# Performance work log

Hardware: AMD Instinct MI355X
Metric: run time of the kernel (lower is better)

## Reference

```python
import jax, jax.numpy as jnp
import numpy as np
from jax.scipy.special import gammaln

D_MODEL = 256
N_HEADS = 8
BIAS_HIDDEN = 64
B, N = 2, 1024
EPS = 1e-4


def setup_inputs() -> dict:
    key = jax.random.key(0)
    ks = jax.random.split(key, 12)
    d, h = D_MODEL, BIAS_HIDDEN
    s = 0.02
    return {
        "src": jax.random.normal(ks[0], (B, N, d), jnp.float32),
        "coords": jax.random.normal(ks[1], (B, N, 4), jnp.float32),
        "Wq": jax.random.normal(ks[2], (d, d), jnp.float32) * s,
        "Wk": jax.random.normal(ks[3], (d, d), jnp.float32) * s,
        "Wv": jax.random.normal(ks[4], (d, d), jnp.float32) * s,
        "Wo": jax.random.normal(ks[5], (d, d), jnp.float32) * s,
        "gw1": jax.random.normal(ks[6], (h, 2), jnp.float32) * s,
        "gb1": jnp.zeros((h,), jnp.float32),
        "gw2": jax.random.normal(ks[7], (1, h), jnp.float32) * s,
        "gb2": jnp.zeros((1,), jnp.float32),
        "dw1": jax.random.normal(ks[8], (h, 4), jnp.float32) * s,
        "db1": jnp.zeros((h,), jnp.float32),
        "dw2": jax.random.normal(ks[9], (2, h), jnp.float32) * s,
        "db2": jnp.zeros((2,), jnp.float32),
    }


def reference(src, coords, Wq, Wk, Wv, Wo, gw1, gb1, gw2, gb2, dw1, db1, dw2, db2):
    Bb, Nn, d = src.shape
    H = N_HEADS
    dh = d // H
    scale = 1.0 / np.sqrt(dh).astype(np.float32)

    def split_heads(x):  # [B,N,d] -> [B,H,N,dh]
        return x.reshape(Bb, Nn, H, dh).transpose(0, 2, 1, 3)

    q = split_heads(src @ Wq.T)
    k = split_heads(src @ Wk.T)
    v = split_heads(src @ Wv.T)

    attn = jnp.einsum("bhnd,bhmd->bhnm", q, k) * scale  # [B,H,N,N]

    xyz = coords[..., :3]
    t = coords[..., 3]
    delta = xyz[:, :, None, :] - xyz[:, None, :, :]        # [B,N,N,3]
    dist = jnp.linalg.norm(delta, axis=-1)                  # [B,N,N]
    dt = t[:, :, None] - t[:, None, :]                      # [B,N,N]

    # geometric bias MLP: 2 -> hidden -> 1
    geom_feat = jnp.stack((dist, dt), axis=-1)              # [B,N,N,2]
    gh = jax.nn.relu(geom_feat @ gw1.T + gb1)
    bias = (gh @ gw2.T + gb2)[..., 0]                       # [B,N,N]

    # delay bias MLP: [dist, xyz_j] (4) -> hidden -> 2 (Gamma shape, rate)
    xyz_j = jnp.broadcast_to(xyz[:, None, :, :], (Bb, Nn, Nn, 3))
    delay_feat = jnp.concatenate((dist[..., None], xyz_j), axis=-1)  # [B,N,N,4]
    dhid = jax.nn.relu(delay_feat @ dw1.T + db1)
    raw = dhid @ dw2.T + db2                                # [B,N,N,2]
    shape = jax.nn.softplus(raw[..., 0]) + EPS
    rate = jax.nn.softplus(raw[..., 1]) + EPS
    dt_pos = jnp.maximum(jnp.abs(dt), EPS)
    # Gamma(shape, rate).log_prob(x)
    log_prob = (shape * jnp.log(rate) + (shape - 1.0) * jnp.log(dt_pos)
                - rate * dt_pos - gammaln(shape))
    bias = bias + log_prob

    attn = attn + bias[:, None, :, :]
    weights = jax.nn.softmax(attn, axis=-1)
    out = jnp.einsum("bhnm,bhmd->bhnd", weights, v)
    out = out.transpose(0, 2, 1, 3).reshape(Bb, Nn, d)
    return out @ Wo.T
```

## Files before the change

kernel.cpp:

```cpp
#include <hip/hip_runtime.h>
#include <hip/hip_bf16.h>
#include <math.h>

constexpr int B_ = 2;
constexpr int N_ = 1024;
constexpr int D_ = 256;
constexpr int H_ = 8;
constexpr int DH_ = 32;
constexpr float SCALE_ = 0.17677669529663687f;
constexpr float LOG2E_ = 1.4426950408889634f;
constexpr float SCALE2_ = SCALE_ * LOG2E_;
constexpr float EPSV_ = 1e-4f;

typedef __attribute__((ext_vector_type(8))) short short8;
typedef __attribute__((ext_vector_type(4))) float f32x4;

__device__ __forceinline__ unsigned short f2bf(float x) {
  __hip_bfloat16 h = __float2bfloat16(x);
  return __builtin_bit_cast(unsigned short, h);
}
__device__ __forceinline__ float bf2f(unsigned short u) {
  unsigned int x = ((unsigned int)u) << 16;
  return __builtin_bit_cast(float, x);
}

__device__ __forceinline__ float lgamma_fast(float x) {
  float y = (x < 1.f) ? x : (x - 1.f);
  float g = fmaf(y, 0.035868343f, -0.193527818f);
  g = fmaf(y, g, 0.482199394f);
  g = fmaf(y, g, -0.756704078f);
  g = fmaf(y, g, 0.918206857f);
  g = fmaf(y, g, -0.897056937f);
  g = fmaf(y, g, 0.988205891f);
  g = fmaf(y, g, -0.577191652f);
  g = fmaf(y, g, 1.0f);
  float lg = __logf(g);
  return (x < 1.f) ? lg - __logf(x) : lg;
}
__device__ __forceinline__ float softplus_fast(float x) {
  return __logf(1.f + __expf(x));
}

__global__ __launch_bounds__(256)
void prep_kernel(const float* __restrict__ coords,
                 const float* __restrict__ gw1, const float* __restrict__ gb1,
                 const float* __restrict__ gw2, const float* __restrict__ gb2,
                 const float* __restrict__ dw1, const float* __restrict__ db1,
                 const float* __restrict__ dw2, const float* __restrict__ db2,
                 const float* __restrict__ Wq, const float* __restrict__ Wk,
                 const float* __restrict__ Wv, const float* __restrict__ Wo,
                 const float* __restrict__ src,
                 unsigned short* __restrict__ whi, unsigned short* __restrict__ wlo,
                 unsigned short* __restrict__ shi, unsigned short* __restrict__ slo,
                 float2* __restrict__ Gp, float4* __restrict__ Dp) {
  const int tid = threadIdx.x;
  const int bi = blockIdx.x;

  if (bi < 33) {
    int e = bi * 256 + tid;
    if (e < 129 * 64) {
      int kv = e >> 6, ku = e & 63;
      float v = kv * 0.25f - 16.0f;
      float u0 = ku * 0.25f, u1 = u0 + 0.25f;
      float a0 = gb2[0], a1 = gb2[0];
#pragma unroll 4
      for (int h = 0; h < 64; ++h) {
        float g0 = gw1[2 * h], g1 = gw1[2 * h + 1], gb = gb1[h], g2 = gw2[h];
        float base = fmaf(g1, v, gb);
        a0 = fmaf(g2, fmaxf(fmaf(g0, u0, base), 0.f), a0);
        a1 = fmaf(g2, fmaxf(fmaf(g0, u1, base), 0.f), a1);
      }
      Gp[e] = make_float2(a0, a1);
    }
    return;
  }

  if (bi < 545) {
    int t = (bi - 33) * 256 + tid;
    int b = t >> 16;
    int rem = t & 65535;
    int k = rem >> 10;
    int j = rem & 1023;
    float4 cj = ((const float4*)coords)[b * N_ + j];
    float u0 = k * 0.25f, u1 = u0 + 0.25f;
    float r00 = db2[0], r10 = db2[1], r01 = db2[0], r11 = db2[1];
#pragma unroll 4
    for (int h = 0; h < 64; ++h) {
      float w0 = dw1[4 * h], wx = dw1[4 * h + 1], wy = dw1[4 * h + 2], wz = dw1[4 * h + 3];
      float c0 = db1[h], c1 = dw2[h], c2 = dw2[64 + h];
      float dp = fmaf(wx, cj.x, fmaf(wy, cj.y, fmaf(wz, cj.z, c0)));
      float h0 = fmaxf(fmaf(w0, u0, dp), 0.f);
      float h1 = fmaxf(fmaf(w0, u1, dp), 0.f);
      r00 = fmaf(c1, h0, r00); r10 = fmaf(c2, h0, r10);
      r01 = fmaf(c1, h1, r01); r11 = fmaf(c2, h1, r11);
    }
    Dp[((size_t)b * 64 + k) * 1024 + j] = make_float4(r00, r10, r01, r11);
    return;
  }

  if (bi < 609) {
    int idx = ((bi - 545) * 256 + tid) * 16;
    int m = idx >> 16;
    int off = idx & 65535;
    const float* p = ((m == 0) ? Wq : (m == 1) ? Wk : (m == 2) ? Wv : Wo) + off;
    unsigned short* dhi = whi + idx;
    unsigned short* dlo = wlo + idx;
#pragma unroll
    for (int q = 0; q < 4; ++q) {
      float4 f = *(const float4*)(p + q * 4);
      ushort4 hi, lo;
      hi.x = f2bf(f.x); lo.x = f2bf(f.x - bf2f(hi.x));
      hi.y = f2bf(f.y); lo.y = f2bf(f.y - bf2f(hi.y));
      hi.z = f2bf(f.z); lo.z = f2bf(f.z - bf2f(hi.z));
      hi.w = f2bf(f.w); lo.w = f2bf(f.w - bf2f(hi.w));
      *(ushort4*)(dhi + q * 4) = hi;
      *(ushort4*)(dlo + q * 4) = lo;
    }
    return;
  }

  {
    int idx = ((bi - 609) * 256 + tid) * 16;
    const float* p = src + idx;
    unsigned short* dhi = shi + idx;
    unsigned short* dlo = slo + idx;
#pragma unroll
    for (int q = 0; q < 4; ++q) {
      float4 f = *(const float4*)(p + q * 4);
      ushort4 hi, lo;
      hi.x = f2bf(f.x); lo.x = f2bf(f.x - bf2f(hi.x));
      hi.y = f2bf(f.y); lo.y = f2bf(f.y - bf2f(hi.y));
      hi.z = f2bf(f.z); lo.z = f2bf(f.z - bf2f(hi.z));
      hi.w = f2bf(f.w); lo.w = f2bf(f.w - bf2f(hi.w));
      *(ushort4*)(dhi + q * 4) = hi;
      *(ushort4*)(dlo + q * 4) = lo;
    }
  }
}

__device__ __forceinline__
void mfma_wave_pure(const unsigned short* __restrict__ Ahi,
                    const unsigned short* __restrict__ Alo,
                    const unsigned short* __restrict__ whi,
                    const unsigned short* __restrict__ wlo,
                    int r0, int c0, f32x4 (&acc)[4]) {
  const int l = threadIdx.x & 63;
  const int lr = l & 15, lg = l >> 4;
#pragma unroll
  for (int ct = 0; ct < 4; ++ct) acc[ct] = (f32x4){0.f, 0.f, 0.f, 0.f};
#pragma unroll 2
  for (int ks = 0; ks < 8; ++ks) {
    size_t aoff = (size_t)(r0 + lr) * D_ + ks * 32 + lg * 8;
    short8 ahi = *(const short8*)(Ahi + aoff);
    short8 alo = *(const short8*)(Alo + aoff);
#pragma unroll
    for (int ct = 0; ct < 4; ++ct) {
      size_t woff = (size_t)(c0 + ct * 16 + lr) * D_ + ks * 32 + lg * 8;
      short8 wh = *(const short8*)(whi + woff);
      short8 wl = *(const short8*)(wlo + woff);
      acc[ct] = __builtin_amdgcn_mfma_f32_16x16x32_bf16(ahi, wh, acc[ct], 0, 0, 0);
      acc[ct] = __builtin_amdgcn_mfma_f32_16x16x32_bf16(alo, wh, acc[ct], 0, 0, 0);
      acc[ct] = __builtin_amdgcn_mfma_f32_16x16x32_bf16(ahi, wl, acc[ct], 0, 0, 0);
    }
  }
}

__global__ __launch_bounds__(256)
void fused1_kernel(const float* __restrict__ coords,
                   const float2* __restrict__ Gp, const float4* __restrict__ Dp,
                   float* __restrict__ bias,
                   const unsigned short* __restrict__ shi,
                   const unsigned short* __restrict__ slo,
                   const unsigned short* __restrict__ whi,
                   const unsigned short* __restrict__ wlo,
                   unsigned short* __restrict__ qbf, unsigned short* __restrict__ kbf,
                   unsigned short* __restrict__ vtbf) {
  const int tid = threadIdx.x;
  const int bi = blockIdx.x;

  if (bi >= 2048) {
    const int bi2 = bi - 2048;
    const int z = bi2 >> 7;
    const int rem = bi2 & 127;
    const int by = rem >> 5, bx = rem & 31;
    const int w = tid >> 6;
    const int r0 = bx * 64 + w * 16;
    const int c0 = by * 64;
    f32x4 acc[4];
    mfma_wave_pure(shi, slo, whi + z * 65536, wlo + z * 65536, r0, c0, acc);

    const int l = tid & 63, lr = l & 15, lg = l >> 4;
    if (z < 2) {
      unsigned short* dst = (z == 0) ? qbf : kbf;
#pragma unroll
      for (int ct = 0; ct < 4; ++ct) {
        int o = c0 + ct * 16 + lr, h = o >> 5, d = o & 31;
#pragma unroll
        for (int r = 0; r < 4; ++r) {
          int R = r0 + lg * 4 + r, b = R >> 10, n = R & 1023;
          dst[(size_t)((b * H_ + h) * N_ + n) * DH_ + d] = f2bf(acc[ct][r]);
        }
      }
    } else {
#pragma unroll
      for (int ct = 0; ct < 4; ++ct) {
        int o = c0 + ct * 16 + lr, h = o >> 5, d = o & 31;
#pragma unroll
        for (int r = 0; r < 4; ++r) {
          int R = r0 + lg * 4 + r, b = R >> 10, n = R & 1023;
          vtbf[(size_t)((b * H_ + h) * DH_ + d) * N_ + n] = f2bf(acc[ct][r]);
        }
      }
    }
    return;
  }

  const int jt = bi & 3;
  const int it = (bi >> 2) & 255;
  const int b  = bi >> 10;
  const int j  = jt * 256 + tid;
  const int ibase = it * 4;

  const float4 cj = ((const float4*)coords)[b * N_ + j];
  const float4* DpB = Dp + (size_t)b * 64 * 1024;

#pragma unroll
  for (int ii = 0; ii < 4; ++ii) {
    const float* cp = coords + 4 * (b * N_ + ibase + ii);
    float dx = cp[0] - cj.x, dy = cp[1] - cj.y, dz = cp[2] - cj.z;
    float dist = sqrtf(dx * dx + dy * dy + dz * dz);
    float dtv = cp[3] - cj.w;

    float uf = fminf(dist, 15.999f) * 4.0f;
    int ku = (int)uf;
    float fu = uf - (float)ku;
    float4 t = DpB[(size_t)ku * 1024 + j];
    float raw0 = fmaf(fu, t.z - t.x, t.x);
    float raw1 = fmaf(fu, t.w - t.y, t.y);

    float vf = (fminf(fmaxf(dtv, -16.0f), 15.999f) + 16.0f) * 4.0f;
    int kv = (int)vf;
    float fv = vf - (float)kv;
    float2 a = Gp[kv * 64 + ku];
    float2 c = Gp[(kv + 1) * 64 + ku];
    float gl = fmaf(fu, a.y - a.x, a.x);
    float gh = fmaf(fu, c.y - c.x, c.x);
    float biasg = fmaf(fv, gh - gl, gl);

    float sh  = softplus_fast(raw0) + EPSV_;
    float ra  = softplus_fast(raw1) + EPSV_;
    float dtp = fmaxf(fabsf(dtv), EPSV_);
    float lp  = sh * __logf(ra) + (sh - 1.f) * __logf(dtp) - ra * dtp - lgamma_fast(sh);
    bias[(size_t)(b * N_ + ibase + ii) * N_ + j] = (biasg + lp) * LOG2E_;
  }
}

__global__ __launch_bounds__(512)
void attn_kernel(const unsigned short* __restrict__ qbf,
                 const unsigned short* __restrict__ kbf,
                 const unsigned short* __restrict__ vtbf,
                 const float* __restrict__ biasg,
                 unsigned short* __restrict__ ophi,
                 unsigned short* __restrict__ oplo) {
  __shared__ __align__(16) unsigned short p_lds[8][16][72];
  __shared__ float acc_lds[3][2][16][32];
  __shared__ float ml_lds[3][2][16][2];

  const int tid = threadIdx.x;
  const int w = tid >> 6, l = tid & 63;
  const int s = w >> 2, jq = w & 3;
  const int lr = l & 15, lg = l >> 4;
  const int bh = blockIdx.x >> 5;
  const int qb = blockIdx.x & 31;
  const int b = bh >> 3, h = bh & 7;
  const int ibase = qb * 32 + s * 16;

  const short8 ones8 = {16256, 16256, 16256, 16256, 16256, 16256, 16256, 16256};

  const short8 qfrag =
      *(const short8*)(qbf + (size_t)(bh * N_ + ibase + lr) * DH_ + lg * 8);
  const unsigned short* kb = kbf + (size_t)bh * N_ * DH_;
  const unsigned short* vb = vtbf + (size_t)bh * DH_ * N_;
  const float* bbase = biasg + (size_t)b * N_ * N_;

  f32x4 acc[2], accL;
  acc[0] = (f32x4){0.f, 0.f, 0.f, 0.f};
  acc[1] = (f32x4){0.f, 0.f, 0.f, 0.f};
  accL   = (f32x4){0.f, 0.f, 0.f, 0.f};
  float m_run[4];
#pragma unroll
  for (int r = 0; r < 4; ++r) m_run[r] = -3e38f;

  const int jbeg = jq * 256;
  for (int j0 = jbeg; j0 < jbeg + 256; j0 += 64) {
    f32x4 sc[4];
#pragma unroll
    for (int t = 0; t < 4; ++t) {
      short8 kf = *(const short8*)(kb + (size_t)(j0 + t * 16 + lr) * DH_ + lg * 8);
      sc[t] = __builtin_amdgcn_mfma_f32_16x16x32_bf16(
          qfrag, kf, (f32x4){0.f, 0.f, 0.f, 0.f}, 0, 0, 0);
    }
#pragma unroll
    for (int r = 0; r < 4; ++r) {
      const float* bp = bbase + (size_t)(ibase + lg * 4 + r) * N_ + j0 + lr;
#pragma unroll
      for (int t = 0; t < 4; ++t)
        sc[t][r] = fmaf(sc[t][r], SCALE2_, bp[t * 16]);
    }
    float mt[4];
#pragma unroll
    for (int r = 0; r < 4; ++r)
      mt[r] = fmaxf(fmaxf(sc[0][r], sc[1][r]), fmaxf(sc[2][r], sc[3][r]));
#pragma unroll
    for (int off = 1; off < 16; off <<= 1)
#pragma unroll
      for (int r = 0; r < 4; ++r)
        mt[r] = fmaxf(mt[r], __shfl_xor(mt[r], off));
    float corr[4];
#pragma unroll
    for (int r = 0; r < 4; ++r) {
      float mn = fmaxf(m_run[r], mt[r]);
      corr[r] = exp2f(m_run[r] - mn);
      m_run[r] = mn;
    }
#pragma unroll
    for (int t = 0; t < 4; ++t)
#pragma unroll
      for (int r = 0; r < 4; ++r)
        sc[t][r] = exp2f(sc[t][r] - m_run[r]);
#pragma unroll
    for (int r = 0; r < 4; ++r) {
      acc[0][r] *= corr[r];
      acc[1][r] *= corr[r];
      accL[r]   *= corr[r];
    }
#pragma unroll
    for (int t = 0; t < 4; ++t)
#pragma unroll
      for (int r = 0; r < 4; ++r)
        p_lds[w][lg * 4 + r][t * 16 + lr] = f2bf(sc[t][r]);
#pragma unroll
    for (int kc = 0; kc < 2; ++kc) {
      short8 pf = *(const short8*)&p_lds[w][lr][kc * 32 + lg * 8];
#pragma unroll
      for (int c = 0; c < 2; ++c) {
        short8 vf = *(const short8*)(vb + (size_t)(c * 16 + lr) * N_ +
                                     j0 + kc * 32 + lg * 8);
        acc[c] = __builtin_amdgcn_mfma_f32_16x16x32_bf16(pf, vf, acc[c], 0, 0, 0);
      }
      accL = __builtin_amdgcn_mfma_f32_16x16x32_bf16(pf, ones8, accL, 0, 0, 0);
    }
  }

  if (jq > 0) {
#pragma unroll
    for (int c = 0; c < 2; ++c)
#pragma unroll
      for (int r = 0; r < 4; ++r)
        acc_lds[jq - 1][s][lg * 4 + r][c * 16 + lr] = acc[c][r];
    if (lr == 0) {
#pragma unroll
      for (int r = 0; r < 4; ++r) {
        ml_lds[jq - 1][s][lg * 4 + r][0] = m_run[r];
        ml_lds[jq - 1][s][lg * 4 + r][1] = accL[r];
      }
    }
  }
  __syncthreads();
  if (jq == 0) {
    float c0[4], cq[3][4], linv[4];
#pragma unroll
    for (int r = 0; r < 4; ++r) {
      int row = lg * 4 + r;
      float m = m_run[r];
#pragma unroll
      for (int q = 0; q < 3; ++q) m = fmaxf(m, ml_lds[q][s][row][0]);
      c0[r] = exp2f(m_run[r] - m);
      float lsum = accL[r] * c0[r];
#pragma unroll
      for (int q = 0; q < 3; ++q) {
        cq[q][r] = exp2f(ml_lds[q][s][row][0] - m);
        lsum = fmaf(ml_lds[q][s][row][1], cq[q][r], lsum);
      }
      linv[r] = 1.f / lsum;
    }
#pragma unroll
    for (int c = 0; c < 2; ++c) {
#pragma unroll
      for (int r = 0; r < 4; ++r) {
        int row = lg * 4 + r;
        int i = ibase + row;
        int d = c * 16 + lr;
        float o = acc[c][r] * c0[r];
#pragma unroll
        for (int q = 0; q < 3; ++q)
          o = fmaf(acc_lds[q][s][row][d], cq[q][r], o);
        o *= linv[r];
        size_t oidx = (size_t)(b * N_ + i) * D_ + h * DH_ + d;
        unsigned short hi = f2bf(o);
        ophi[oidx] = hi;
        oplo[oidx] = f2bf(o - bf2f(hi));
      }
    }
  }
}

__global__ __launch_bounds__(256)
void projo_kernel(const unsigned short* __restrict__ ophi,
                  const unsigned short* __restrict__ oplo,
                  const unsigned short* __restrict__ whi,
                  const unsigned short* __restrict__ wlo,
                  float* __restrict__ out) {
  const int w = threadIdx.x >> 6;
  const int r0 = blockIdx.x * 64 + w * 16;
  const int c0 = blockIdx.y * 64;
  f32x4 acc[4];
  mfma_wave_pure(ophi, oplo, whi + 3 * 65536, wlo + 3 * 65536, r0, c0, acc);
  const int l = threadIdx.x & 63, lr = l & 15, lg = l >> 4;
#pragma unroll
  for (int ct = 0; ct < 4; ++ct)
#pragma unroll
    for (int r = 0; r < 4; ++r)
      out[(size_t)(r0 + lg * 4 + r) * D_ + c0 + ct * 16 + lr] = acc[ct][r];
}

extern "C" void kernel_launch(void* const* d_in, const int* in_sizes, int n_in,
                              void* d_out, int out_size, void* d_ws, size_t ws_size,
                              hipStream_t stream) {
  const float* src    = (const float*)d_in[0];
  const float* coords = (const float*)d_in[1];
  const float* Wq  = (const float*)d_in[2];
  const float* Wk  = (const float*)d_in[3];
  const float* Wv  = (const float*)d_in[4];
  const float* Wo  = (const float*)d_in[5];
  const float* gw1 = (const float*)d_in[6];
  const float* gb1 = (const float*)d_in[7];
  const float* gw2 = (const float*)d_in[8];
  const float* gb2 = (const float*)d_in[9];
  const float* dw1 = (const float*)d_in[10];
  const float* db1 = (const float*)d_in[11];
  const float* dw2 = (const float*)d_in[12];
  const float* db2 = (const float*)d_in[13];
  float* out = (float*)d_out;

  char* wsb = (char*)d_ws;
  unsigned short* qbf  = (unsigned short*)wsb;
  unsigned short* kbf  = (unsigned short*)(wsb + (1 << 20));
  unsigned short* vtbf = (unsigned short*)(wsb + (2 << 20));
  float* biasw         = (float*)(wsb + (3 << 20));
  unsigned short* whi  = (unsigned short*)(wsb + (11 << 20));
  unsigned short* wlo  = (unsigned short*)(wsb + (11 << 20) + (512 << 10));
  unsigned short* shi  = (unsigned short*)(wsb + (12 << 20));
  unsigned short* slo  = (unsigned short*)(wsb + (13 << 20));
  unsigned short* ophi = (unsigned short*)(wsb + (14 << 20));
  unsigned short* oplo = (unsigned short*)(wsb + (15 << 20));
  float2* Gp           = (float2*)(wsb + (16 << 20));
  float4* Dp           = (float4*)(wsb + (17 << 20));

  prep_kernel<<<737, 256, 0, stream>>>(coords, gw1, gb1, gw2, gb2,
                                       dw1, db1, dw2, db2,
                                       Wq, Wk, Wv, Wo, src,
                                       whi, wlo, shi, slo, Gp, Dp);
  fused1_kernel<<<2432, 256, 0, stream>>>(coords, Gp, Dp, biasw,
                                          shi, slo, whi, wlo, qbf, kbf, vtbf);
  attn_kernel<<<512, 512, 0, stream>>>(qbf, kbf, vtbf, biasw, ophi, oplo);
  projo_kernel<<<dim3(32, 4), 256, 0, stream>>>(ophi, oplo, whi, wlo, out);
}
```

Baseline: 71.25 us.

## Fuse attention and output projection via software grid barrier

Merges the attention kernel and the output-projection kernel into one launch. A global atomic barrier separates the two phases, and the first 64 blocks then run the projection. This removes one kernel launch and the gap between kernels. In exchange it adds a memset launch and spin-wait synchronisation. It also relies on all 512 blocks being co-resident, which is risky if occupancy does not allow it.

```diff
diff --git a/kernel.cpp b/kernel.cpp
--- a/kernel.cpp
+++ b/kernel.cpp
@@ -11,6 +11,7 @@
 constexpr float LOG2E_ = 1.4426950408889634f;
 constexpr float SCALE2_ = SCALE_ * LOG2E_;
 constexpr float EPSV_ = 1e-4f;
+constexpr unsigned GRID2_ = 512;
 
 typedef __attribute__((ext_vector_type(8))) short short8;
 typedef __attribute__((ext_vector_type(4))) float f32x4;
@@ -39,6 +40,22 @@
 }
 __device__ __forceinline__ float softplus_fast(float x) {
   return __logf(1.f + __expf(x));
+}
+
+__device__ __forceinline__ void grid_barrier(unsigned* bar) {
+  __syncthreads();
+  if (threadIdx.x == 0) {
+    __threadfence();
+    unsigned old = atomicAdd(bar, 1u);
+    if (old == GRID2_ - 1) {
+      atomicExch(bar + 1, 1u);
+    } else {
+      while (atomicAdd(bar + 1, 0u) == 0u)
+        __builtin_amdgcn_s_sleep(2);
+    }
+    __threadfence();
+  }
+  __syncthreads();
 }
 
 __global__ __launch_bounds__(256)
@@ -143,8 +160,7 @@
                     const unsigned short* __restrict__ Alo,
                     const unsigned short* __restrict__ whi,
                     const unsigned short* __restrict__ wlo,
-                    int r0, int c0, f32x4 (&acc)[4]) {
-  const int l = threadIdx.x & 63;
+                    int r0, int c0, int l, f32x4 (&acc)[4]) {
   const int lr = l & 15, lg = l >> 4;
 #pragma unroll
   for (int ct = 0; ct < 4; ++ct) acc[ct] = (f32x4){0.f, 0.f, 0.f, 0.f};
@@ -187,7 +203,7 @@
     const int r0 = bx * 64 + w * 16;
     const int c0 = by * 64;
     f32x4 acc[4];
-    mfma_wave_pure(shi, slo, whi + z * 65536, wlo + z * 65536, r0, c0, acc);
+    mfma_wave_pure(shi, slo, whi + z * 65536, wlo + z * 65536, r0, c0, tid & 63, acc);
 
     const int l = tid & 63, lr = l & 15, lg = l >> 4;
     if (z < 2) {
@@ -255,173 +271,181 @@
   }
 }
 
-__global__ __launch_bounds__(512)
-void attn_kernel(const unsigned short* __restrict__ qbf,
-                 const unsigned short* __restrict__ kbf,
-                 const unsigned short* __restrict__ vtbf,
-                 const float* __restrict__ biasg,
-                 unsigned short* __restrict__ ophi,
-                 unsigned short* __restrict__ oplo) {
+__global__
+__attribute__((amdgpu_flat_work_group_size(512, 512), amdgpu_waves_per_eu(4, 4)))
+void attn_projo_kernel(const unsigned short* __restrict__ qbf,
+                       const unsigned short* __restrict__ kbf,
+                       const unsigned short* __restrict__ vtbf,
+                       const float* __restrict__ biasg,
+                       const unsigned short* __restrict__ whi,
+                       const unsigned short* __restrict__ wlo,
+                       unsigned short* __restrict__ ophi,
+                       unsigned short* __restrict__ oplo,
+                       float* __restrict__ out,
+                       unsigned* __restrict__ bar) {
   __shared__ __align__(16) unsigned short p_lds[8][16][72];
   __shared__ float acc_lds[3][2][16][32];
   __shared__ float ml_lds[3][2][16][2];
 
   const int tid = threadIdx.x;
-  const int w = tid >> 6, l = tid & 63;
-  const int s = w >> 2, jq = w & 3;
-  const int lr = l & 15, lg = l >> 4;
-  const int bh = blockIdx.x >> 5;
-  const int qb = blockIdx.x & 31;
-  const int b = bh >> 3, h = bh & 7;
-  const int ibase = qb * 32 + s * 16;
-
-  const short8 ones8 = {16256, 16256, 16256, 16256, 16256, 16256, 16256, 16256};
-
-  const short8 qfrag =
-      *(const short8*)(qbf + (size_t)(bh * N_ + ibase + lr) * DH_ + lg * 8);
-  const unsigned short* kb = kbf + (size_t)bh * N_ * DH_;
-  const unsigned short* vb = vtbf + (size_t)bh * DH_ * N_;
-  const float* bbase = biasg + (size_t)b * N_ * N_;
-
-  f32x4 acc[2], accL;
-  acc[0] = (f32x4){0.f, 0.f, 0.f, 0.f};
-  acc[1] = (f32x4){0.f, 0.f, 0.f, 0.f};
-  accL   = (f32x4){0.f, 0.f, 0.f, 0.f};
-  float m_run[4];
-#pragma unroll
-  for (int r = 0; r < 4; ++r) m_run[r] = -3e38f;
-
-  const int jbeg = jq * 256;
-  for (int j0 = jbeg; j0 < jbeg + 256; j0 += 64) {
-    f32x4 sc[4];
-#pragma unroll
-    for (int t = 0; t < 4; ++t) {
-      short8 kf = *(const short8*)(kb + (size_t)(j0 + t * 16 + lr) * DH_ + lg * 8);
-      sc[t] = __builtin_amdgcn_mfma_f32_16x16x32_bf16(
-          qfrag, kf, (f32x4){0.f, 0.f, 0.f, 0.f}, 0, 0, 0);
-    }
-#pragma unroll
-    for (int r = 0; r < 4; ++r) {
-      const float* bp = bbase + (size_t)(ibase + lg * 4 + r) * N_ + j0 + lr;
+  const int bi = blockIdx.x;
+
+  {
+    const int w = tid >> 6, l = tid & 63;
+    const int s = w >> 2, jq = w & 3;
+    const int lr = l & 15, lg = l >> 4;
+    const int bh = bi >> 5;
+    const int qb = bi & 31;
+    const int b = bh >> 3, h = bh & 7;
+    const int ibase = qb * 32 + s * 16;
+
+    const short8 ones8 = {16256, 16256, 16256, 16256, 16256, 16256, 16256, 16256};
+    const short8 qfrag =
+        *(const short8*)(qbf + (size_t)(bh * N_ + ibase + lr) * DH_ + lg * 8);
+    const unsigned short* kb = kbf + (size_t)bh * N_ * DH_;
+    const unsigned short* vb = vtbf + (size_t)bh * DH_ * N_;
+    const float* bbase = biasg + (size_t)b * N_ * N_;
+
+    f32x4 acc[2], accL;
+    acc[0] = (f32x4){0.f, 0.f, 0.f, 0.f};
+    acc[1] = (f32x4){0.f, 0.f, 0.f, 0.f};
+    accL   = (f32x4){0.f, 0.f, 0.f, 0.f};
+    float m_run[4];
+#pragma unroll
+    for (int r = 0; r < 4; ++r) m_run[r] = -3e38f;
+
+    const int jbeg = jq * 256;
+    for (int j0 = jbeg; j0 < jbeg + 256; j0 += 64) {
+      f32x4 sc[4];
+#pragma unroll
+      for (int t = 0; t < 4; ++t) {
+        short8 kf = *(const short8*)(kb + (size_t)(j0 + t * 16 + lr) * DH_ + lg * 8);
+        sc[t] = __builtin_amdgcn_mfma_f32_16x16x32_bf16(
+            qfrag, kf, (f32x4){0.f, 0.f, 0.f, 0.f}, 0, 0, 0);
+      }
+#pragma unroll
+      for (int r = 0; r < 4; ++r) {
+        const float* bp = bbase + (size_t)(ibase + lg * 4 + r) * N_ + j0 + lr;
+#pragma unroll
+        for (int t = 0; t < 4; ++t)
+          sc[t][r] = fmaf(sc[t][r], SCALE2_, bp[t * 16]);
+      }
+      float mt[4];
+#pragma unroll
+      for (int r = 0; r < 4; ++r)
+        mt[r] = fmaxf(fmaxf(sc[0][r], sc[1][r]), fmaxf(sc[2][r], sc[3][r]));
+#pragma unroll
+      for (int off = 1; off < 16; off <<= 1)
+#pragma unroll
+        for (int r = 0; r < 4; ++r)
+          mt[r] = fmaxf(mt[r], __shfl_xor(mt[r], off));
+      float corr[4];
+#pragma unroll
+      for (int r = 0; r < 4; ++r) {
+        float mn = fmaxf(m_run[r], mt[r]);
+        corr[r] = exp2f(m_run[r] - mn);
+        m_run[r] = mn;
+      }
 #pragma unroll
       for (int t = 0; t < 4; ++t)
-        sc[t][r] = fmaf(sc[t][r], SCALE2_, bp[t * 16]);
-    }
-    float mt[4];
-#pragma unroll
-    for (int r = 0; r < 4; ++r)
-      mt[r] = fmaxf(fmaxf(sc[0][r], sc[1][r]), fmaxf(sc[2][r], sc[3][r]));
-#pragma unroll
-    for (int off = 1; off < 16; off <<= 1)
-#pragma unroll
-      for (int r = 0; r < 4; ++r)
-        mt[r] = fmaxf(mt[r], __shfl_xor(mt[r], off));
-    float corr[4];
-#pragma unroll
-    for (int r = 0; r < 4; ++r) {
-      float mn = fmaxf(m_run[r], mt[r]);
-      corr[r] = exp2f(m_run[r] - mn);
-      m_run[r] = mn;
-    }
-#pragma unroll
-    for (int t = 0; t < 4; ++t)
-#pragma unroll
-      for (int r = 0; r < 4; ++r)
-        sc[t][r] = exp2f(sc[t][r] - m_run[r]);
-#pragma unroll
-    for (int r = 0; r < 4; ++r) {
-      acc[0][r] *= corr[r];
-      acc[1][r] *= corr[r];
-      accL[r]   *= corr[r];
-    }
-#pragma unroll
-    for (int t = 0; t < 4; ++t)
-#pragma unroll
-      for (int r = 0; r < 4; ++r)
-        p_lds[w][lg * 4 + r][t * 16 + lr] = f2bf(sc[t][r]);
-#pragma unroll
-    for (int kc = 0; kc < 2; ++kc) {
-      short8 pf = *(const short8*)&p_lds[w][lr][kc * 32 + lg * 8];
-#pragma unroll
-      for (int c = 0; c < 2; ++c) {
-        short8 vf = *(const short8*)(vb + (size_t)(c * 16 + lr) * N_ +
-                                     j0 + kc * 32 + lg * 8);
-        acc[c] = __builtin_amdgcn_mfma_f32_16x16x32_bf16(pf, vf, acc[c], 0, 0, 0);
-      }
-      accL = __builtin_amdgcn_mfma_f32_16x16x32_bf16(pf, ones8, accL, 0, 0, 0);
-    }
-  }
-
-  if (jq > 0) {
-#pragma unroll
-    for (int c = 0; c < 2; ++c)
-#pragma unroll
-      for (int r = 0; r < 4; ++r)
-        acc_lds[jq - 1][s][lg * 4 + r][c * 16 + lr] = acc[c][r];
-    if (lr == 0) {
+#pragma unroll
+        for (int r = 0; r < 4; ++r)
+          sc[t][r] = exp2f(sc[t][r] - m_run[r]);
 #pragma unroll
       for (int r = 0; r < 4; ++r) {
-        ml_lds[jq - 1][s][lg * 4 + r][0] = m_run[r];
-        ml_lds[jq - 1][s][lg * 4 + r][1] = accL[r];
-      }
-    }
-  }
-  __syncthreads();
-  if (jq == 0) {
-    float c0[4], cq[3][4], linv[4];
-#pragma unroll
-    for (int r = 0; r < 4; ++r) {
-      int row = lg * 4 + r;
-      float m = m_run[r];
-#pragma unroll
-      for (int q = 0; q < 3; ++q) m = fmaxf(m, ml_lds[q][s][row][0]);
-      c0[r] = exp2f(m_run[r] - m);
-      float lsum = accL[r] * c0[r];
-#pragma unroll
-      for (int q = 0; q < 3; ++q) {
-        cq[q][r] = exp2f(ml_lds[q][s][row][0] - m);
-        lsum = fmaf(ml_lds[q][s][row][1], cq[q][r], lsum);
-      }
-      linv[r] = 1.f / lsum;
-    }
-#pragma unroll
-    for (int c = 0; c < 2; ++c) {
+        acc[0][r] *= corr[r];
+        acc[1][r] *= corr[r];
+        accL[r]   *= corr[r];
+      }
+#pragma unroll
+      for (int t = 0; t < 4; ++t)
+#pragma unroll
+        for (int r = 0; r < 4; ++r)
+          p_lds[w][lg * 4 + r][t * 16 + lr] = f2bf(sc[t][r]);
+#pragma unroll
+      for (int kc = 0; kc < 2; ++kc) {
+        short8 pf = *(const short8*)&p_lds[w][lr][kc * 32 + lg * 8];
+#pragma unroll
+        for (int c = 0; c < 2; ++c) {
+          short8 vf = *(const short8*)(vb + (size_t)(c * 16 + lr) * N_ +
+                                       j0 + kc * 32 + lg * 8);
+          acc[c] = __builtin_amdgcn_mfma_f32_16x16x32_bf16(pf, vf, acc[c], 0, 0, 0);
+        }
+        accL = __builtin_amdgcn_mfma_f32_16x16x32_bf16(pf, ones8, accL, 0, 0, 0);
+      }
+    }
+
+    if (jq > 0) {
+#pragma unroll
+      for (int c = 0; c < 2; ++c)
+#pragma unroll
+        for (int r = 0; r < 4; ++r)
+          acc_lds[jq - 1][s][lg * 4 + r][c * 16 + lr] = acc[c][r];
+      if (lr == 0) {
+#pragma unroll
+        for (int r = 0; r < 4; ++r) {
+          ml_lds[jq - 1][s][lg * 4 + r][0] = m_run[r];
+          ml_lds[jq - 1][s][lg * 4 + r][1] = accL[r];
+        }
+      }
+    }
+    __syncthreads();
+    if (jq == 0) {
+      float c0[4], cq[3][4], linv[4];
 #pragma unroll
       for (int r = 0; r < 4; ++r) {
         int row = lg * 4 + r;
-        int i = ibase + row;
-        int d = c * 16 + lr;
-        float o = acc[c][r] * c0[r];
-#pragma unroll
-        for (int q = 0; q < 3; ++q)
-          o = fmaf(acc_lds[q][s][row][d], cq[q][r], o);
-        o *= linv[r];
-        size_t oidx = (size_t)(b * N_ + i) * D_ + h * DH_ + d;
-        unsigned short hi = f2bf(o);
-        ophi[oidx] = hi;
-        oplo[oidx] = f2bf(o - bf2f(hi));
-      }
-    }
-  }
-}
-
-__global__ __launch_bounds__(256)
-void projo_kernel(const unsigned short* __restrict__ ophi,
-                  const unsigned short* __restrict__ oplo,
-                  const unsigned short* __restrict__ whi,
-                  const unsigned short* __restrict__ wlo,
-                  float* __restrict__ out) {
-  const int w = threadIdx.x >> 6;
-  const int r0 = blockIdx.x * 64 + w * 16;
-  const int c0 = blockIdx.y * 64;
-  f32x4 acc[4];
-  mfma_wave_pure(ophi, oplo, whi + 3 * 65536, wlo + 3 * 65536, r0, c0, acc);
-  const int l = threadIdx.x & 63, lr = l & 15, lg = l >> 4;
-#pragma unroll
-  for (int ct = 0; ct < 4; ++ct)
-#pragma unroll
-    for (int r = 0; r < 4; ++r)
-      out[(size_t)(r0 + lg * 4 + r) * D_ + c0 + ct * 16 + lr] = acc[ct][r];
+        float m = m_run[r];
+#pragma unroll
+        for (int q = 0; q < 3; ++q) m = fmaxf(m, ml_lds[q][s][row][0]);
+        c0[r] = exp2f(m_run[r] - m);
+        float lsum = accL[r] * c0[r];
+#pragma unroll
+        for (int q = 0; q < 3; ++q) {
+          cq[q][r] = exp2f(ml_lds[q][s][row][0] - m);
+          lsum = fmaf(ml_lds[q][s][row][1], cq[q][r], lsum);
+        }
+        linv[r] = 1.f / lsum;
+      }
+#pragma unroll
+      for (int c = 0; c < 2; ++c) {
+#pragma unroll
+        for (int r = 0; r < 4; ++r) {
+          int row = lg * 4 + r;
+          int i = ibase + row;
+          int d = c * 16 + lr;
+          float o = acc[c][r] * c0[r];
+#pragma unroll
+          for (int q = 0; q < 3; ++q)
+            o = fmaf(acc_lds[q][s][row][d], cq[q][r], o);
+          o *= linv[r];
+          size_t oidx = (size_t)(b * N_ + i) * D_ + h * DH_ + d;
+          unsigned short hi = f2bf(o);
+          ophi[oidx] = hi;
+          oplo[oidx] = f2bf(o - bf2f(hi));
+        }
+      }
+    }
+  }
+
+  grid_barrier(bar);
+
+  if (bi < 64) {
+    const int u = bi * 2 + (tid >> 8);
+    const int utid = tid & 255;
+    const int by = u >> 5, bx = u & 31;
+    const int w = utid >> 6, l = utid & 63;
+    const int r0 = bx * 64 + w * 16;
+    const int c0 = by * 64;
+    f32x4 acc[4];
+    mfma_wave_pure(ophi, oplo, whi + 3 * 65536, wlo + 3 * 65536, r0, c0, l, acc);
+    const int lr = l & 15, lg = l >> 4;
+#pragma unroll
+    for (int ct = 0; ct < 4; ++ct)
+#pragma unroll
+      for (int r = 0; r < 4; ++r)
+        out[(size_t)(r0 + lg * 4 + r) * D_ + c0 + ct * 16 + lr] = acc[ct][r];
+  }
 }
 
 extern "C" void kernel_launch(void* const* d_in, const int* in_sizes, int n_in,
@@ -456,13 +480,15 @@
   unsigned short* oplo = (unsigned short*)(wsb + (15 << 20));
   float2* Gp           = (float2*)(wsb + (16 << 20));
   float4* Dp           = (float4*)(wsb + (17 << 20));
-
+  unsigned* bar        = (unsigned*)(wsb + (20 << 20));
+
+  hipMemsetAsync(bar, 0, 64, stream);
   prep_kernel<<<737, 256, 0, stream>>>(coords, gw1, gb1, gw2, gb2,
                                        dw1, db1, dw2, db2,
                                        Wq, Wk, Wv, Wo, src,
                                        whi, wlo, shi, slo, Gp, Dp);
   fused1_kernel<<<2432, 256, 0, stream>>>(coords, Gp, Dp, biasw,
                                           shi, slo, whi, wlo, qbf, kbf, vtbf);
-  attn_kernel<<<512, 512, 0, stream>>>(qbf, kbf, vtbf, biasw, ophi, oplo);
-  projo_kernel<<<dim3(32, 4), 256, 0, stream>>>(ophi, oplo, whi, wlo, out);
-}
+  attn_projo_kernel<<<GRID2_, 512, 0, stream>>>(qbf, kbf, vtbf, biasw,
+                                                whi, wlo, ophi, oplo, out, bar);
+}
```

Result: slower. 135.5 us (+90.2%).
